# Kernel tuning notes

Measured on AMD Instinct MI355X. Metric: run time of the kernel, lower is better.

The kernel has to match this reference:

```python
import jax, jax.numpy as jnp
import numpy as np

D_MODEL = 2048
N_HEADS = 16
HEAD_DIM = D_MODEL // N_HEADS
D_FF = 8192
B, T = 2, 2048
LN_EPS = 1e-5


def layer_norm(x, g, b):
    mu = jnp.mean(x, axis=-1, keepdims=True)
    var = jnp.mean(jnp.square(x - mu), axis=-1, keepdims=True)
    return (x - mu) * jax.lax.rsqrt(var + LN_EPS) * g + b


def setup_inputs() -> dict:
    key = jax.random.key(0)
    ks = jax.random.split(key, 8)
    s = 0.02
    return {
        "x": jax.random.normal(ks[0], (B, T, D_MODEL), dtype=jnp.float32),
        "ln1_g": jnp.ones((D_MODEL,), jnp.float32),
        "ln1_b": jnp.zeros((D_MODEL,), jnp.float32),
        "ln2_g": jnp.ones((D_MODEL,), jnp.float32),
        "ln2_b": jnp.zeros((D_MODEL,), jnp.float32),
        "w_qkv": jax.random.normal(ks[1], (3 * D_MODEL, D_MODEL), jnp.float32) * s,
        "w_out": jax.random.normal(ks[2], (D_MODEL, D_MODEL), jnp.float32) * s,
        "w_up": jax.random.normal(ks[3], (D_FF, D_MODEL), jnp.float32) * s,
        "b_up": jnp.zeros((D_FF,), jnp.float32),
        "w_down": jax.random.normal(ks[4], (D_MODEL, D_FF), jnp.float32) * s,
        "b_down": jnp.zeros((D_MODEL,), jnp.float32),
    }


def reference(x, ln1_g, ln1_b, ln2_g, ln2_b, w_qkv, w_out, w_up, b_up, w_down, b_down):
    b, t, c = x.shape
    # --- attention (pre-norm) ---
    h = layer_norm(x, ln1_g, ln1_b)
    qkv = h @ w_qkv.T                                  # [B,T,3C]
    q, k, v = jnp.split(qkv, 3, axis=-1)
    # [B,H,T,Dh]
    q = q.reshape(b, t, N_HEADS, HEAD_DIM).transpose(0, 2, 1, 3)
    k = k.reshape(b, t, N_HEADS, HEAD_DIM).transpose(0, 2, 1, 3)
    v = v.reshape(b, t, N_HEADS, HEAD_DIM).transpose(0, 2, 1, 3)
    scale = 1.0 / np.sqrt(HEAD_DIM).astype(np.float32)
    attn = jnp.einsum("bhqd,bhkd->bhqk", q, k) * scale
    causal = jnp.tril(jnp.ones((t, t), dtype=bool))
    attn = jnp.where(causal, attn, jnp.float32(-jnp.inf))
    attn = jax.nn.softmax(attn, axis=-1)
    out = jnp.einsum("bhqk,bhkd->bhqd", attn, v)
    out = out.transpose(0, 2, 1, 3).reshape(b, t, c)
    x = x + out @ w_out.T
    # --- FFN (pre-norm, GeLU exact) ---
    h = layer_norm(x, ln2_g, ln2_b)
    h = jax.nn.gelu(h @ w_up.T + b_up, approximate=False)
    x = x + h @ w_down.T + b_down
    return x
```

## Files before the change

kernel.cpp:

```cpp
#include <hip/hip_runtime.h>
#include <cstdint>
#include <cstddef>

using u16 = unsigned short;
typedef __attribute__((ext_vector_type(8))) __bf16 bf16x8;
typedef __attribute__((ext_vector_type(4))) float f32x4;

__device__ inline u16 f2bf(float f) {
  union { float f; unsigned u; } v; v.f = f;
  unsigned r = (v.u + 0x7fffu + ((v.u >> 16) & 1u)) >> 16;
  return (u16)r;
}

#define GLDS(g, s) __builtin_amdgcn_global_load_lds( \
    (__attribute__((address_space(1))) void*)(g), \
    (__attribute__((address_space(3))) void*)(s), 16, 0, 0)

__global__ __launch_bounds__(256) void cvt_bf16(const float* __restrict__ in,
                                                u16* __restrict__ out, int n8) {
  int i = blockIdx.x * 256 + threadIdx.x;
  if (i >= n8) return;
  float4 v0 = *(const float4*)&in[(size_t)i * 8];
  float4 v1 = *(const float4*)&in[(size_t)i * 8 + 4];
  union { u16 u[8]; uint4 q; } pk;
  pk.u[0] = f2bf(v0.x); pk.u[1] = f2bf(v0.y); pk.u[2] = f2bf(v0.z); pk.u[3] = f2bf(v0.w);
  pk.u[4] = f2bf(v1.x); pk.u[5] = f2bf(v1.y); pk.u[6] = f2bf(v1.z); pk.u[7] = f2bf(v1.w);
  *(uint4*)&out[(size_t)i * 8] = pk.q;
}

__global__ __launch_bounds__(256) void ln_bf16(const float* __restrict__ x,
                                               const float* __restrict__ g,
                                               const float* __restrict__ bsh,
                                               u16* __restrict__ out) {
  __shared__ float red[8];
  int tid = threadIdx.x;
  int lane = tid & 63, w = tid >> 6;
  size_t row = blockIdx.x;
  const float* xr = x + row * 2048;
  float4 v0 = *(const float4*)&xr[tid * 8];
  float4 v1 = *(const float4*)&xr[tid * 8 + 4];
  float s = v0.x + v0.y + v0.z + v0.w + v1.x + v1.y + v1.z + v1.w;
  float s2 = v0.x*v0.x + v0.y*v0.y + v0.z*v0.z + v0.w*v0.w
           + v1.x*v1.x + v1.y*v1.y + v1.z*v1.z + v1.w*v1.w;
#pragma unroll
  for (int m = 1; m < 64; m <<= 1) { s += __shfl_xor(s, m); s2 += __shfl_xor(s2, m); }
  if (lane == 0) { red[w] = s; red[w + 4] = s2; }
  __syncthreads();
  s = red[0] + red[1] + red[2] + red[3];
  s2 = red[4] + red[5] + red[6] + red[7];
  float mu = s * (1.0f / 2048.0f);
  float var = s2 * (1.0f / 2048.0f) - mu * mu;
  float rs = rsqrtf(var + 1e-5f);
  float4 g0 = *(const float4*)&g[tid * 8];
  float4 g1 = *(const float4*)&g[tid * 8 + 4];
  float4 b0 = *(const float4*)&bsh[tid * 8];
  float4 b1 = *(const float4*)&bsh[tid * 8 + 4];
  float xv[8] = {v0.x, v0.y, v0.z, v0.w, v1.x, v1.y, v1.z, v1.w};
  float gv[8] = {g0.x, g0.y, g0.z, g0.w, g1.x, g1.y, g1.z, g1.w};
  float bv[8] = {b0.x, b0.y, b0.z, b0.w, b1.x, b1.y, b1.z, b1.w};
  union { u16 u[8]; uint4 q; } pk;
#pragma unroll
  for (int j = 0; j < 8; j++) pk.u[j] = f2bf((xv[j] - mu) * rs * gv[j] + bv[j]);
  *(uint4*)&out[row * 2048 + tid * 8] = pk.q;
}

__global__ __launch_bounds__(256) void combine2(const float* __restrict__ a,
                                                const float* __restrict__ b,
                                                const float* __restrict__ resid,
                                                const float* __restrict__ bias,
                                                float* __restrict__ out, int n4) {
  int stride = gridDim.x * 256;
  for (int i = blockIdx.x * 256 + threadIdx.x; i < n4; i += stride) {
    float4 va = ((const float4*)a)[i];
    float4 vb = ((const float4*)b)[i];
    float4 vr = ((const float4*)resid)[i];
    float4 o;
    o.x = va.x + vb.x + vr.x; o.y = va.y + vb.y + vr.y;
    o.z = va.z + vb.z + vr.z; o.w = va.w + vb.w + vr.w;
    if (bias) {
      int col0 = (i * 4) & 2047;
      float4 bb = *(const float4*)&bias[col0];
      o.x += bb.x; o.y += bb.y; o.z += bb.z; o.w += bb.w;
    }
    ((float4*)out)[i] = o;
  }
}

template <int EPI, int LDK, int KLEN, bool SPLITK>
__global__ __launch_bounds__(512) void gemm256(
    const u16* __restrict__ A, const u16* __restrict__ B,
    int M, int N,
    const float* __restrict__ bias,
    float* __restrict__ outf, u16* __restrict__ outh,
    int xc, int chr, int chc) {
  __shared__ u16 lds[65536];
  constexpr int NT = KLEN / 64;
  int tid = threadIdx.x;
  int lane = tid & 63, wid = tid >> 6;
  int wr = wid >> 2, wc = wid & 3;
  int lr = lane & 15, lg = lane >> 4;

  int nbx = N >> 8;
  int sub = blockIdx.x;
  if (SPLITK) {
    int half = (M >> 8) * nbx;
    if (sub >= half) {
      sub -= half;
      A += (size_t)KLEN;
      B += (size_t)KLEN;
      outf += (size_t)M * N;
    }
  }
  int xcd = sub & 7, slot = sub >> 3;
  int rr = slot / chc, cc = slot - rr * chc;
  int by = (xcd / xc) * chr + rr;
  int bx = (xcd - (xcd / xc) * xc) * chc + cc;
  size_t bm = (size_t)by * 256, bn = (size_t)bx * 256;

  const u16* Ablk = A + bm * LDK;
  const u16* Bblk = B + bn * LDK;

  int sA[2], sB[2];
#pragma unroll
  for (int c = 0; c < 2; ++c) {
    int s = tid + c * 512;
    int wrr = s >> 9, r2 = (s >> 3) & 63, g = s & 7;
    sA[c] = (wrr * 128 + r2) * LDK + ((g ^ (r2 & 7)) * 8);
    int rb = s >> 3, gb = s & 7;
    sB[c] = rb * LDK + ((gb ^ (rb & 7)) * 8);
  }
  int aoff[2], boff[2];
#pragma unroll
  for (int kk = 0; kk < 2; ++kk) {
    int gs = ((kk * 4 + lg) ^ (lr & 7)) * 8;
    aoff[kk] = wr * 4096 + lr * 64 + gs;
    boff[kk] = 32768 + (wc >> 1) * 8192 + (wc & 1) * 4096 + lr * 64 + gs;
  }

  f32x4 acc[8][4];
#pragma unroll
  for (int m = 0; m < 8; ++m)
#pragma unroll
    for (int n = 0; n < 4; ++n) acc[m][n] = (f32x4){0.f, 0.f, 0.f, 0.f};

  bf16x8 af[4][2], bfr[2][2][2];

#define STAGE_A(bb, hh, tt) do { \
    GLDS(Ablk + (hh) * 64 * LDK + (tt) * 64 + sA[0], &lds[(bb) * 16384 + (hh) * 8192 + tid * 8]); \
    GLDS(Ablk + (hh) * 64 * LDK + (tt) * 64 + sA[1], &lds[(bb) * 16384 + (hh) * 8192 + 4096 + tid * 8]); \
  } while (0)
#define STAGE_B(bb, hh, tt) do { \
    GLDS(Bblk + (hh) * 128 * LDK + (tt) * 64 + sB[0], &lds[32768 + (bb) * 16384 + (hh) * 8192 + tid * 8]); \
    GLDS(Bblk + (hh) * 128 * LDK + (tt) * 64 + sB[1], &lds[32768 + (bb) * 16384 + (hh) * 8192 + 4096 + tid * 8]); \
  } while (0)
#define LOAD_A(bb, mh) do { \
    _Pragma("unroll") for (int mq = 0; mq < 4; ++mq) { \
      af[mq][0] = *(const bf16x8*)&lds[(bb) * 16384 + (mh) * 8192 + mq * 1024 + aoff[0]]; \
      af[mq][1] = *(const bf16x8*)&lds[(bb) * 16384 + (mh) * 8192 + mq * 1024 + aoff[1]]; \
    } } while (0)
#define LOAD_B(bb, nh) do { \
    _Pragma("unroll") for (int nq = 0; nq < 2; ++nq) { \
      bfr[nh][nq][0] = *(const bf16x8*)&lds[(bb) * 16384 + (nh) * 2048 + nq * 1024 + boff[0]]; \
      bfr[nh][nq][1] = *(const bf16x8*)&lds[(bb) * 16384 + (nh) * 2048 + nq * 1024 + boff[1]]; \
    } } while (0)
#define MFMA_Q(mh, nh) do { \
    __builtin_amdgcn_s_setprio(1); \
    _Pragma("unroll") for (int kk = 0; kk < 2; ++kk) \
    _Pragma("unroll") for (int mq = 0; mq < 4; ++mq) \
    _Pragma("unroll") for (int nq = 0; nq < 2; ++nq) \
      acc[(mh)*4+mq][(nh)*2+nq] = __builtin_amdgcn_mfma_f32_16x16x32_bf16(af[mq][kk], bfr[nh][nq][kk], acc[(mh)*4+mq][(nh)*2+nq], 0, 0, 0); \
    __builtin_amdgcn_s_setprio(0); \
  } while (0)
#define BAR __builtin_amdgcn_s_barrier()
#define LGKM0 asm volatile("s_waitcnt lgkmcnt(0)" ::: "memory")
#define LGKM8 asm volatile("s_waitcnt lgkmcnt(8)" ::: "memory")
#define VM6 asm volatile("s_waitcnt vmcnt(6)" ::: "memory")
#define VM0 asm volatile("s_waitcnt vmcnt(0)" ::: "memory")

  STAGE_A(0, 0, 0); STAGE_A(0, 1, 0); STAGE_B(0, 0, 0); STAGE_B(0, 1, 0);
  STAGE_A(1, 0, 1); STAGE_B(1, 0, 1); STAGE_B(1, 1, 1);
  VM6;
  BAR;

  for (int t = 0; t + 3 < NT; t += 2) {
    LOAD_A(0, 0); LOAD_B(0, 0); STAGE_A(1, 1, t + 1); LGKM8;
    BAR; LGKM0; MFMA_Q(0, 0); BAR;
    LOAD_B(0, 1); STAGE_A(0, 0, t + 2);
    BAR; LGKM0; MFMA_Q(0, 1); BAR;
    LOAD_A(0, 1); STAGE_B(0, 0, t + 2);
    BAR; LGKM0; MFMA_Q(1, 0); BAR;
    STAGE_B(0, 1, t + 2);
    BAR; MFMA_Q(1, 1); VM6; BAR;
    LOAD_A(1, 0); LOAD_B(1, 0); STAGE_A(0, 1, t + 2); LGKM8;
    BAR; LGKM0; MFMA_Q(0, 0); BAR;
    LOAD_B(1, 1); STAGE_A(1, 0, t + 3);
    BAR; LGKM0; MFMA_Q(0, 1); BAR;
    LOAD_A(1, 1); STAGE_B(1, 0, t + 3);
    BAR; LGKM0; MFMA_Q(1, 0); BAR;
    STAGE_B(1, 1, t + 3);
    BAR; MFMA_Q(1, 1); VM6; BAR;
  }

  STAGE_A(1, 1, NT - 1);

  VM0; BAR;
  LOAD_A(0, 0); LOAD_B(0, 0); LOAD_B(0, 1);
  MFMA_Q(0, 0); MFMA_Q(0, 1);
  LOAD_A(0, 1);
  MFMA_Q(1, 0); MFMA_Q(1, 1);
  LOAD_A(1, 0); LOAD_B(1, 0); LOAD_B(1, 1);
  MFMA_Q(0, 0); MFMA_Q(0, 1);
  LOAD_A(1, 1);
  MFMA_Q(1, 0); MFMA_Q(1, 1);

#undef STAGE_A
#undef STAGE_B
#undef LOAD_A
#undef LOAD_B
#undef MFMA_Q
#undef BAR
#undef LGKM0
#undef LGKM8
#undef VM6
#undef VM0

  size_t row0 = bm + wr * 128, col0 = bn + wc * 64;
#pragma unroll
  for (int mg = 0; mg < 8; ++mg) {
#pragma unroll
    for (int ng = 0; ng < 4; ++ng) {
#pragma unroll
      for (int r = 0; r < 4; ++r) {
        size_t row = row0 + (mg >> 2) * 64 + (mg & 3) * 16 + lg * 4 + r;
        size_t col = col0 + (ng >> 1) * 32 + (ng & 1) * 16 + lr;
        size_t idx = row * (size_t)N + col;
        float v = acc[mg][ng][r];
        if (EPI == 0) {
          outh[idx] = f2bf(v);
        } else if (EPI == 2) {
          v += bias[col];
          outh[idx] = f2bf(0.5f * v * (1.0f + erff(v * 0.70710678118654752f)));
        } else if (EPI == 4) {
          outf[idx] = v;
        }
      }
    }
  }
}

__global__ __launch_bounds__(256) void vtrans(const u16* __restrict__ qkv,
                                              u16* __restrict__ vt) {
  __shared__ u16 tile[32][33];
  int tx = threadIdx.x & 31, ty = threadIdx.x >> 5;
  int t0 = blockIdx.x * 32, d0 = blockIdx.y * 32, bh = blockIdx.z;
  int b = bh >> 4, h = bh & 15;
  const u16* src = qkv + (size_t)b * 2048 * 6144 + 4096 + h * 128 + d0;
#pragma unroll
  for (int i = 0; i < 4; i++)
    tile[ty + i * 8][tx] = src[(size_t)(t0 + ty + i * 8) * 6144 + tx];
  __syncthreads();
  u16* dst = vt + (size_t)bh * 128 * 2048 + (size_t)d0 * 2048 + t0;
#pragma unroll
  for (int i = 0; i < 4; i++)
    dst[(size_t)(ty + i * 8) * 2048 + tx] = tile[tx][ty + i * 8];
}

__device__ inline void stage_kv(const u16* __restrict__ ktok, const u16* __restrict__ vbase,
                                int k0, u16* kb, u16* vb, int tid) {
#pragma unroll
  for (int c = 0; c < 4; ++c) {
    int s = c * 256 + tid;
    int r = s >> 4, g = s & 15;
    const u16* src = ktok + (size_t)(k0 + r) * 6144 + ((g ^ (r & 7)) * 8);
    GLDS(src, &kb[s * 8]);
  }
#pragma unroll
  for (int c = 0; c < 4; ++c) {
    int s = c * 256 + tid;
    int d = s >> 3, g = s & 7;
    const u16* src = vbase + (size_t)d * 2048 + k0 + ((g ^ (d & 7)) * 8);
    GLDS(src, &vb[s * 8]);
  }
}

__global__ __launch_bounds__(256) void attn_fwd(const u16* __restrict__ qkv,
                                                const u16* __restrict__ vt,
                                                u16* __restrict__ outh) {
  __shared__ u16 kbuf[2][8192];
  __shared__ u16 vbuf[2][8192];
  __shared__ u16 p_lds[4][1024];
  int tid = threadIdx.x, lane = tid & 63, w = tid >> 6;
  int lr = lane & 15, lg = lane >> 4;
  int bh = blockIdx.x, p = blockIdx.y;
  int b = bh >> 4, h = bh & 15;
  const float scale = 0.08838834764831845f;
  const u16* tokbase = qkv + (size_t)b * 2048 * 6144;
  const u16* ktok = tokbase + 2048 + h * 128;
  const u16* vbase = vt + (size_t)bh * 262144;
  u16* pl = p_lds[w];

  for (int half = 0; half < 2; ++half) {
    int qt = (half == 0) ? p : 31 - p;
    int qbase = qt * 64 + w * 16;
    int nt = qt + 1;

    bf16x8 qf[4];
    const u16* qrow_ptr = tokbase + (size_t)(qbase + lr) * 6144 + h * 128;
#pragma unroll
    for (int kk = 0; kk < 4; kk++) qf[kk] = *(const bf16x8*)&qrow_ptr[kk * 32 + lg * 8];

    f32x4 o[8];
#pragma unroll
    for (int d = 0; d < 8; d++) o[d] = (f32x4){0.f, 0.f, 0.f, 0.f};
    float mrow[4] = {-1e30f, -1e30f, -1e30f, -1e30f};
    float lsum[4] = {0.f, 0.f, 0.f, 0.f};

    int cur = 0;
    stage_kv(ktok, vbase, 0, kbuf[0], vbuf[0], tid);
    __syncthreads();

    for (int t = 0; t < nt; ++t) {
      int k0 = t * 64;
      if (t + 1 < nt) stage_kv(ktok, vbase, k0 + 64, kbuf[cur ^ 1], vbuf[cur ^ 1], tid);
      const u16* kb = kbuf[cur];
      const u16* vb = vbuf[cur];

      f32x4 s[4];
#pragma unroll
      for (int c = 0; c < 4; c++) s[c] = (f32x4){0.f, 0.f, 0.f, 0.f};
#pragma unroll
      for (int kk = 0; kk < 4; kk++) {
#pragma unroll
        for (int c = 0; c < 4; c++) {
          bf16x8 kf = *(const bf16x8*)&kb[(c * 16 + lr) * 128 + (((kk * 4 + lg) ^ (lr & 7)) * 8)];
          s[c] = __builtin_amdgcn_mfma_f32_16x16x32_bf16(qf[kk], kf, s[c], 0, 0, 0);
        }
      }

      float mt[4];
#pragma unroll
      for (int r = 0; r < 4; r++) {
        int qrow = qbase + lg * 4 + r;
        float m = -1e30f;
#pragma unroll
        for (int c = 0; c < 4; c++) {
          int key = k0 + c * 16 + lr;
          float v = (key <= qrow) ? s[c][r] * scale : -1e30f;
          s[c][r] = v;
          m = fmaxf(m, v);
        }
        mt[r] = m;
      }
#pragma unroll
      for (int msk = 1; msk < 16; msk <<= 1)
#pragma unroll
        for (int r = 0; r < 4; r++) mt[r] = fmaxf(mt[r], __shfl_xor(mt[r], msk));
      float al[4], ps[4];
#pragma unroll
      for (int r = 0; r < 4; r++) {
        float mn = fmaxf(mrow[r], mt[r]);
        al[r] = __expf(mrow[r] - mn);
        mrow[r] = mn;
        float sum = 0.f;
#pragma unroll
        for (int c = 0; c < 4; c++) {
          float pv = __expf(s[c][r] - mn);
          s[c][r] = pv;
          sum += pv;
        }
        ps[r] = sum;
      }
#pragma unroll
      for (int msk = 1; msk < 16; msk <<= 1)
#pragma unroll
        for (int r = 0; r < 4; r++) ps[r] += __shfl_xor(ps[r], msk);
#pragma unroll
      for (int r = 0; r < 4; r++) lsum[r] = lsum[r] * al[r] + ps[r];
#pragma unroll
      for (int d = 0; d < 8; d++)
#pragma unroll
        for (int r = 0; r < 4; r++) o[d][r] *= al[r];

#pragma unroll
      for (int r = 0; r < 4; r++) {
        int prow = lg * 4 + r;
#pragma unroll
        for (int c = 0; c < 4; c++) {
          int gw = (c * 2 + (lr >> 3)) ^ (prow & 7);
          pl[prow * 64 + gw * 8 + (lr & 7)] = f2bf(s[c][r]);
        }
      }
      asm volatile("s_waitcnt lgkmcnt(0)" ::: "memory");
      bf16x8 pa[2];
#pragma unroll
      for (int ks = 0; ks < 2; ks++)
        pa[ks] = *(const bf16x8*)&pl[lr * 64 + (((ks * 4 + lg) ^ (lr & 7)) * 8)];
#pragma unroll
      for (int dt = 0; dt < 8; dt++) {
#pragma unroll
        for (int ks = 0; ks < 2; ks++) {
          bf16x8 vf = *(const bf16x8*)&vb[(dt * 16 + lr) * 64 + (((ks * 4 + lg) ^ (lr & 7)) * 8)];
          o[dt] = __builtin_amdgcn_mfma_f32_16x16x32_bf16(pa[ks], vf, o[dt], 0, 0, 0);
        }
      }
      __syncthreads();
      cur ^= 1;
    }

    float inv[4];
#pragma unroll
    for (int r = 0; r < 4; r++) inv[r] = 1.0f / lsum[r];
    u16* ob = outh + (size_t)(b * 2048 + qbase) * 2048 + h * 128;
#pragma unroll
    for (int dt = 0; dt < 8; dt++)
#pragma unroll
      for (int r = 0; r < 4; r++)
        ob[(size_t)(lg * 4 + r) * 2048 + dt * 16 + lr] = f2bf(o[dt][r] * inv[r]);
  }
}

extern "C" void kernel_launch(void* const* d_in, const int* in_sizes, int n_in,
                              void* d_out, int out_size, void* d_ws, size_t ws_size,
                              hipStream_t stream) {
  const float* x      = (const float*)d_in[0];
  const float* ln1_g  = (const float*)d_in[1];
  const float* ln1_b  = (const float*)d_in[2];
  const float* ln2_g  = (const float*)d_in[3];
  const float* ln2_b  = (const float*)d_in[4];
  const float* w_qkv  = (const float*)d_in[5];
  const float* w_out  = (const float*)d_in[6];
  const float* w_up   = (const float*)d_in[7];
  const float* b_up   = (const float*)d_in[8];
  const float* w_down = (const float*)d_in[9];
  const float* b_down = (const float*)d_in[10];
  float* outp = (float*)d_out;

  char* ws = (char*)d_ws;
  u16* w_qkv_bf  = (u16*)(ws + 0);
  u16* w_out_bf  = (u16*)(ws + 25165824);
  u16* w_up_bf   = (u16*)(ws + 33554432);
  u16* w_down_bf = (u16*)(ws + 67108864);
  u16* hb        = (u16*)(ws + 100663296);
  u16* qkvb      = (u16*)(ws + 117440512);
  u16* vtb       = (u16*)(ws + 167772160);
  u16* ub        = (u16*)(ws + 117440512);
  float* x1      = (float*)(ws + 184549376);
  float* oPart   = (float*)(ws + 117440512);
  float* dPart   = (float*)(ws + 0);

  cvt_bf16<<<6144, 256, 0, stream>>>(w_qkv, w_qkv_bf, 1572864);
  cvt_bf16<<<2048, 256, 0, stream>>>(w_out, w_out_bf, 524288);
  cvt_bf16<<<8192, 256, 0, stream>>>(w_up, w_up_bf, 2097152);
  cvt_bf16<<<8192, 256, 0, stream>>>(w_down, w_down_bf, 2097152);

  ln_bf16<<<4096, 256, 0, stream>>>(x, ln1_g, ln1_b, hb);
  gemm256<0, 2048, 2048, false><<<384, 512, 0, stream>>>(hb, w_qkv_bf, 4096, 6144,
                                                         nullptr, nullptr, qkvb, 4, 8, 6);
  vtrans<<<dim3(64, 4, 32), 256, 0, stream>>>(qkvb, vtb);
  attn_fwd<<<dim3(32, 16), 256, 0, stream>>>(qkvb, vtb, hb);
  gemm256<4, 2048, 1024, true><<<256, 512, 0, stream>>>(hb, w_out_bf, 4096, 2048,
                                                        nullptr, oPart, nullptr, 2, 4, 4);
  combine2<<<2048, 256, 0, stream>>>(oPart, oPart + 8388608, x, nullptr, x1, 2097152);

  ln_bf16<<<4096, 256, 0, stream>>>(x1, ln2_g, ln2_b, hb);
  gemm256<2, 2048, 2048, false><<<512, 512, 0, stream>>>(hb, w_up_bf, 4096, 8192,
                                                         b_up, nullptr, ub, 4, 8, 8);
  gemm256<4, 8192, 4096, true><<<256, 512, 0, stream>>>(ub, w_down_bf, 4096, 2048,
                                                        nullptr, dPart, nullptr, 2, 4, 4);
  combine2<<<2048, 256, 0, stream>>>(dPart, dPart + 8388608, x1, b_down, outp, 2097152);
}
```

Baseline: 723.4 us.

## Restructure GEMM main loop into two barrier phases with double A fragments

Rewrites the bf16 GEMM main loop so each K-step's LDS fragments (both A halves and all B) are read up front into separate register sets, then all 16 MFMA groups run across two phases. Each phase has a single barrier instead of four, and the explicit lgkmcnt waits are replaced with sched_barrier fences that let the compiler place the waits. Global-to-LDS staging is regrouped so it overlaps the MFMA work. The aim is to cut barrier and wait overhead and improve overlap of MFMA with memory traffic. In exchange it needs more VGPRs for the extra A fragment set, which can raise register pressure and lower occupancy.

```diff
diff --git a/kernel.cpp b/kernel.cpp
--- a/kernel.cpp
+++ b/kernel.cpp
@@ -143,7 +143,7 @@
 #pragma unroll
     for (int n = 0; n < 4; ++n) acc[m][n] = (f32x4){0.f, 0.f, 0.f, 0.f};
 
-  bf16x8 af[4][2], bfr[2][2][2];
+  bf16x8 af[4][2], ag[4][2], bfr[2][2][2];
 
 #define STAGE_A(bb, hh, tt) do { \
     GLDS(Ablk + (hh) * 64 * LDK + (tt) * 64 + sA[0], &lds[(bb) * 16384 + (hh) * 8192 + tid * 8]); \
@@ -153,74 +153,78 @@
     GLDS(Bblk + (hh) * 128 * LDK + (tt) * 64 + sB[0], &lds[32768 + (bb) * 16384 + (hh) * 8192 + tid * 8]); \
     GLDS(Bblk + (hh) * 128 * LDK + (tt) * 64 + sB[1], &lds[32768 + (bb) * 16384 + (hh) * 8192 + 4096 + tid * 8]); \
   } while (0)
-#define LOAD_A(bb, mh) do { \
+#define RD_A0(bb) do { \
     _Pragma("unroll") for (int mq = 0; mq < 4; ++mq) { \
-      af[mq][0] = *(const bf16x8*)&lds[(bb) * 16384 + (mh) * 8192 + mq * 1024 + aoff[0]]; \
-      af[mq][1] = *(const bf16x8*)&lds[(bb) * 16384 + (mh) * 8192 + mq * 1024 + aoff[1]]; \
+      af[mq][0] = *(const bf16x8*)&lds[(bb) * 16384 + mq * 1024 + aoff[0]]; \
+      af[mq][1] = *(const bf16x8*)&lds[(bb) * 16384 + mq * 1024 + aoff[1]]; \
     } } while (0)
-#define LOAD_B(bb, nh) do { \
+#define RD_A1(bb) do { \
+    _Pragma("unroll") for (int mq = 0; mq < 4; ++mq) { \
+      ag[mq][0] = *(const bf16x8*)&lds[(bb) * 16384 + 8192 + mq * 1024 + aoff[0]]; \
+      ag[mq][1] = *(const bf16x8*)&lds[(bb) * 16384 + 8192 + mq * 1024 + aoff[1]]; \
+    } } while (0)
+#define RD_B2(bb, nh) do { \
     _Pragma("unroll") for (int nq = 0; nq < 2; ++nq) { \
       bfr[nh][nq][0] = *(const bf16x8*)&lds[(bb) * 16384 + (nh) * 2048 + nq * 1024 + boff[0]]; \
       bfr[nh][nq][1] = *(const bf16x8*)&lds[(bb) * 16384 + (nh) * 2048 + nq * 1024 + boff[1]]; \
     } } while (0)
-#define MFMA_Q(mh, nh) do { \
+#define MFMA_H(FR, mh, nh) do { \
     __builtin_amdgcn_s_setprio(1); \
     _Pragma("unroll") for (int kk = 0; kk < 2; ++kk) \
     _Pragma("unroll") for (int mq = 0; mq < 4; ++mq) \
     _Pragma("unroll") for (int nq = 0; nq < 2; ++nq) \
-      acc[(mh)*4+mq][(nh)*2+nq] = __builtin_amdgcn_mfma_f32_16x16x32_bf16(af[mq][kk], bfr[nh][nq][kk], acc[(mh)*4+mq][(nh)*2+nq], 0, 0, 0); \
+      acc[(mh)*4+mq][(nh)*2+nq] = __builtin_amdgcn_mfma_f32_16x16x32_bf16(FR[mq][kk], bfr[nh][nq][kk], acc[(mh)*4+mq][(nh)*2+nq], 0, 0, 0); \
     __builtin_amdgcn_s_setprio(0); \
   } while (0)
 #define BAR __builtin_amdgcn_s_barrier()
-#define LGKM0 asm volatile("s_waitcnt lgkmcnt(0)" ::: "memory")
-#define LGKM8 asm volatile("s_waitcnt lgkmcnt(8)" ::: "memory")
+#define SB0 __builtin_amdgcn_sched_barrier(0)
 #define VM6 asm volatile("s_waitcnt vmcnt(6)" ::: "memory")
 #define VM0 asm volatile("s_waitcnt vmcnt(0)" ::: "memory")
 
   STAGE_A(0, 0, 0); STAGE_A(0, 1, 0); STAGE_B(0, 0, 0); STAGE_B(0, 1, 0);
   STAGE_A(1, 0, 1); STAGE_B(1, 0, 1); STAGE_B(1, 1, 1);
   VM6;
-  BAR;
+  BAR; SB0;
 
   for (int t = 0; t + 3 < NT; t += 2) {
-    LOAD_A(0, 0); LOAD_B(0, 0); STAGE_A(1, 1, t + 1); LGKM8;
-    BAR; LGKM0; MFMA_Q(0, 0); BAR;
-    LOAD_B(0, 1); STAGE_A(0, 0, t + 2);
-    BAR; LGKM0; MFMA_Q(0, 1); BAR;
-    LOAD_A(0, 1); STAGE_B(0, 0, t + 2);
-    BAR; LGKM0; MFMA_Q(1, 0); BAR;
-    STAGE_B(0, 1, t + 2);
-    BAR; MFMA_Q(1, 1); VM6; BAR;
-    LOAD_A(1, 0); LOAD_B(1, 0); STAGE_A(0, 1, t + 2); LGKM8;
-    BAR; LGKM0; MFMA_Q(0, 0); BAR;
-    LOAD_B(1, 1); STAGE_A(1, 0, t + 3);
-    BAR; LGKM0; MFMA_Q(0, 1); BAR;
-    LOAD_A(1, 1); STAGE_B(1, 0, t + 3);
-    BAR; LGKM0; MFMA_Q(1, 0); BAR;
-    STAGE_B(1, 1, t + 3);
-    BAR; MFMA_Q(1, 1); VM6; BAR;
-  }
-
+    RD_A0(0); RD_B2(0, 0); RD_B2(0, 1); RD_A1(0);
+    STAGE_A(1, 1, t + 1);
+    MFMA_H(af, 0, 0);
+    MFMA_H(af, 0, 1);
+    BAR; SB0;
+    STAGE_A(0, 0, t + 2); STAGE_B(0, 0, t + 2); STAGE_B(0, 1, t + 2);
+    MFMA_H(ag, 1, 0);
+    MFMA_H(ag, 1, 1);
+    VM6;
+    BAR; SB0;
+    RD_A0(1); RD_B2(1, 0); RD_B2(1, 1); RD_A1(1);
+    STAGE_A(0, 1, t + 2);
+    MFMA_H(af, 0, 0);
+    MFMA_H(af, 0, 1);
+    BAR; SB0;
+    STAGE_A(1, 0, t + 3); STAGE_B(1, 0, t + 3); STAGE_B(1, 1, t + 3);
+    MFMA_H(ag, 1, 0);
+    MFMA_H(ag, 1, 1);
+    VM6;
+    BAR; SB0;
+  }
+
+  RD_A0(0); RD_B2(0, 0); RD_B2(0, 1); RD_A1(0);
   STAGE_A(1, 1, NT - 1);
-
-  VM0; BAR;
-  LOAD_A(0, 0); LOAD_B(0, 0); LOAD_B(0, 1);
-  MFMA_Q(0, 0); MFMA_Q(0, 1);
-  LOAD_A(0, 1);
-  MFMA_Q(1, 0); MFMA_Q(1, 1);
-  LOAD_A(1, 0); LOAD_B(1, 0); LOAD_B(1, 1);
-  MFMA_Q(0, 0); MFMA_Q(0, 1);
-  LOAD_A(1, 1);
-  MFMA_Q(1, 0); MFMA_Q(1, 1);
+  MFMA_H(af, 0, 0); MFMA_H(af, 0, 1); MFMA_H(ag, 1, 0); MFMA_H(ag, 1, 1);
+  VM0;
+  BAR; SB0;
+  RD_A0(1); RD_B2(1, 0); RD_B2(1, 1); RD_A1(1);
+  MFMA_H(af, 0, 0); MFMA_H(af, 0, 1); MFMA_H(ag, 1, 0); MFMA_H(ag, 1, 1);
 
 #undef STAGE_A
 #undef STAGE_B
-#undef LOAD_A
-#undef LOAD_B
-#undef MFMA_Q
+#undef RD_A0
+#undef RD_A1
+#undef RD_B2
+#undef MFMA_H
 #undef BAR
-#undef LGKM0
-#undef LGKM8
+#undef SB0
 #undef VM6
 #undef VM0
 
```

New measurement: 723.3 us. About the same (-0.0%).
